# Performance work log

Hardware: AMD Instinct MI355X
Metric: run time of the kernel (lower is better)

The kernel has to match this reference:

```python
import jax, jax.numpy as jnp
import numpy as np
import math

BS, SEQ, HID = 1, 2048, 2048
NH, NKV, HD = 32, 8, 64
BASE = 10000.0


def rotate_half(x):
    x1, x2 = x[..., : x.shape[-1] // 2], x[..., x.shape[-1] // 2 :]
    return jnp.concatenate((-x2, x1), axis=-1)


def setup_inputs() -> dict:
    key = jax.random.key(0)
    ks = jax.random.split(key, 6)
    s = 0.02
    return {
        "x": jax.random.normal(ks[0], (BS, SEQ, HID), dtype=jnp.float32),
        "attention_mask": jnp.zeros((BS, SEQ), dtype=jnp.float32),
        "position_ids": jnp.broadcast_to(jnp.arange(SEQ, dtype=jnp.int64 if jax.config.jax_enable_x64 else jnp.int32), (BS, SEQ)),
        "wq": jax.random.normal(ks[1], (HID, NH * HD), dtype=jnp.float32) * s,
        "wk": jax.random.normal(ks[2], (HID, NKV * HD), dtype=jnp.float32) * s,
        "wv": jax.random.normal(ks[3], (HID, NKV * HD), dtype=jnp.float32) * s,
        "wo": jax.random.normal(ks[4], (NH * HD, HID), dtype=jnp.float32) * s,
    }


def reference(x, attention_mask, position_ids, wq, wk, wv, wo):
    bs, seq, _ = x.shape
    groups = NH // NKV

    q = (x @ wq).reshape(bs, seq, NH, HD).transpose(0, 2, 1, 3)   # [b,H,S,D]
    k = (x @ wk).reshape(bs, seq, NKV, HD).transpose(0, 2, 1, 3)  # [b,Hkv,S,D]
    v = (x @ wv).reshape(bs, seq, NKV, HD).transpose(0, 2, 1, 3)

    # rotary embedding
    inv_freq = 1.0 / (BASE ** (jnp.arange(0, HD, 2, dtype=jnp.float32) / HD))  # [D/2]
    freqs = position_ids.astype(jnp.float32)[:, :, None] * inv_freq[None, None, :]  # [b,S,D/2]
    emb = jnp.concatenate((freqs, freqs), axis=-1)               # [b,S,D]
    cos = jnp.cos(emb)[:, None, :, :].astype(x.dtype)            # [b,1,S,D]
    sin = jnp.sin(emb)[:, None, :, :].astype(x.dtype)
    q = q * cos + rotate_half(q) * sin
    k = k * cos + rotate_half(k) * sin

    # repeat_kv (GQA expand)
    k = jnp.repeat(k, groups, axis=1)  # [b,H,S,D]
    v = jnp.repeat(v, groups, axis=1)

    scores = jnp.einsum("bhqd,bhkd->bhqk", q, k) / math.sqrt(HD)
    scores = scores + attention_mask[:, None, None, :]
    attn = jax.nn.softmax(scores.astype(jnp.float32), axis=-1).astype(q.dtype)
    out = jnp.einsum("bhqk,bhkd->bhqd", attn, v)                 # [b,H,S,D]
    out = out.transpose(0, 2, 1, 3).reshape(bs, seq, NH * HD)
    return out @ wo
```

## Files before the change

### kernel.cpp

```cpp
#include <hip/hip_runtime.h>

#define SEQ 2048
#define HID 2048
#define NH  32
#define NKV 8
#define HD  64

typedef _Float16 f16;
typedef __attribute__((ext_vector_type(4))) _Float16 f16x4;
typedef __attribute__((ext_vector_type(8))) _Float16 f16x8;
typedef __attribute__((ext_vector_type(2))) __fp16   h16x2;
typedef __attribute__((ext_vector_type(4))) float    f32x4;

__device__ __forceinline__ f32x4 mfma_16x16x32(f16x8 a, f16x8 b, f32x4 c) {
    return __builtin_amdgcn_mfma_f32_16x16x32_f16(a, b, c, 0, 0, 0);
}

__device__ __forceinline__ void async16(const void* g, void* l) {
    __builtin_amdgcn_global_load_lds(
        (const __attribute__((address_space(1))) void*)g,
        (__attribute__((address_space(3))) void*)l,
        16, 0, 0);
}

__device__ __forceinline__ void xcd_colmap(int& bx, int& by) {
    int gx = gridDim.x, gy = gridDim.y;
    int nwg = gx * gy;
    int orig = by * gx + bx;
    int q = nwg >> 3, r = nwg & 7;
    int xcd = orig & 7, loc = orig >> 3;
    int wg = (xcd < r ? xcd * (q + 1) : r * (q + 1) + (xcd - r) * q) + loc;
    bx = wg / gy;
    by = wg - bx * gy;
}

__global__ void prep_all(const float* __restrict__ x,
                         const float* __restrict__ wq, const float* __restrict__ wk,
                         const float* __restrict__ wv, const float* __restrict__ wo,
                         f16* __restrict__ xb,
                         f16* __restrict__ Wcat, f16* __restrict__ woT) {
    __shared__ float tile[32][33];
    int z = blockIdx.z;
    int tx = threadIdx.x, ty = threadIdx.y;
    if (z == 4) {
        int idx = (blockIdx.y * 64 + blockIdx.x) * 256 + ty * 32 + tx;
        int i = idx * 4;
        float4 v = *(const float4*)(x + i);
        f16x4 o = { (f16)v.x, (f16)v.y, (f16)v.z, (f16)v.w };
        *(f16x4*)(xb + i) = o;
        return;
    }
    const float* src; f16* dst; int C;
    if      (z == 0) { src = wq; dst = Wcat;                         C = 2048; }
    else if (z == 1) { src = wk; dst = Wcat + (size_t)2048 * 2048;   C = 512;  }
    else if (z == 2) { src = wv; dst = Wcat + (size_t)2560 * 2048;   C = 512;  }
    else             { src = wo; dst = woT;                          C = 2048; }
    int c0 = blockIdx.x * 32, r0 = blockIdx.y * 32;
    if (c0 >= C) return;
#pragma unroll
    for (int i = 0; i < 32; i += 8)
        tile[ty + i][tx] = src[(size_t)(r0 + ty + i) * C + c0 + tx];
    __syncthreads();
#pragma unroll
    for (int i = 0; i < 32; i += 8)
        dst[(size_t)(c0 + ty + i) * 2048 + r0 + tx] = (f16)tile[tx][ty + i];
}

template <int MODE>
__global__ __launch_bounds__(256)
void gemm_bt(const f16* __restrict__ A, const f16* __restrict__ BT,
             float* __restrict__ Cf, f16* __restrict__ Q, f16* __restrict__ Kk,
             f16* __restrict__ VT, const int* __restrict__ pos,
             const float* __restrict__ mask, int N, int K) {
    __shared__ f16 As[2][64 * 64];
    __shared__ f16 Bs[2][128 * 64];
    int t = threadIdx.x;
    int w = t >> 6, lane = t & 63, quad = lane >> 4, l15 = lane & 15;
    int wm = w >> 1, wn = w & 1;
    int bx = blockIdx.x, by = blockIdx.y;
    xcd_colmap(bx, by);
    int m0 = by * 64, n0 = bx * 128;
    int sw = l15 & 7;

    int r8 = lane >> 3;
    int cc = (lane & 7) ^ r8;
    const f16* Ag0 = A  + (size_t)(m0 + w * 16 + r8) * K + cc * 8;
    const f16* Ag1 = Ag0 + (size_t)8 * K;
    const f16* Bg  = BT + (size_t)(n0 + w * 32 + r8) * K + cc * 8;

    f32x4 acc[2][4] = {};

    async16(Ag0, &As[0][w * 1024]);
    async16(Ag1, &As[0][w * 1024 + 512]);
#pragma unroll
    for (int g = 0; g < 4; g++)
        async16(Bg + (size_t)(8 * g) * K, &Bs[0][w * 2048 + g * 512]);
    __syncthreads();

    int b = 0;
    for (int kt = 64; kt <= K; kt += 64) {
        if (kt < K) {
            async16(Ag0 + kt, &As[b ^ 1][w * 1024]);
            async16(Ag1 + kt, &As[b ^ 1][w * 1024 + 512]);
#pragma unroll
            for (int g = 0; g < 4; g++)
                async16(Bg + (size_t)(8 * g) * K + kt, &Bs[b ^ 1][w * 2048 + g * 512]);
        }
        f16x8 af[2][2], bf[4][2];
#pragma unroll
        for (int mi = 0; mi < 2; mi++) {
            int row = wm * 32 + mi * 16 + l15;
#pragma unroll
            for (int kh = 0; kh < 2; kh++)
                af[mi][kh] = *(const f16x8*)(&As[b][row * 64 + ((kh * 4 + quad) ^ sw) * 8]);
        }
#pragma unroll
        for (int ni = 0; ni < 4; ni++) {
            int row = wn * 64 + ni * 16 + l15;
#pragma unroll
            for (int kh = 0; kh < 2; kh++)
                bf[ni][kh] = *(const f16x8*)(&Bs[b][row * 64 + ((kh * 4 + quad) ^ sw) * 8]);
        }
#pragma unroll
        for (int mi = 0; mi < 2; mi++)
#pragma unroll
            for (int ni = 0; ni < 4; ni++) {
                acc[mi][ni] = mfma_16x16x32(af[mi][0], bf[ni][0], acc[mi][ni]);
                acc[mi][ni] = mfma_16x16x32(af[mi][1], bf[ni][1], acc[mi][ni]);
            }
        __syncthreads();
        b ^= 1;
    }

    int rb  = m0 + wm * 32 + quad * 4;
    int cbh = n0 + wn * 64;
    if (MODE == 0) {
        if (cbh < (NH + NKV) * HD) {
            bool isQ = cbh < NH * HD;
            f16* dst = isQ ? (Q  + (size_t)(cbh >> 6) * SEQ * HD)
                           : (Kk + (size_t)((cbh - NH * HD) >> 6) * SEQ * HD);
            float scale = isQ ? 0.18033688011112042f : 1.0f;
            float fr[2];
#pragma unroll
            for (int ni = 0; ni < 2; ni++)
                fr[ni] = __builtin_amdgcn_exp2f(
                    (float)(ni * 16 + l15) * -0.41524101186092029f);
#pragma unroll
            for (int mi = 0; mi < 2; mi++)
#pragma unroll
                for (int r = 0; r < 4; r++) {
                    int row = rb + mi * 16 + r;
                    float pv = (float)pos[row];
#pragma unroll
                    for (int ni = 0; ni < 2; ni++) {
                        float sn, cs;
                        __sincosf(pv * fr[ni], &sn, &cs);
                        float x1 = acc[mi][ni][r], x2 = acc[mi][ni + 2][r];
                        int d = ni * 16 + l15;
                        dst[(size_t)row * HD + d]      = (f16)(scale * (x1 * cs - x2 * sn));
                        dst[(size_t)row * HD + d + 32] = (f16)(scale * (x2 * cs + x1 * sn));
                    }
                }
        } else {
            const float LOG2E = 1.4426950408889634f;
#pragma unroll
            for (int mi = 0; mi < 2; mi++) {
                float4 mv = *(const float4*)(mask + rb + mi * 16);
                float em[4];
#pragma unroll
                for (int r = 0; r < 4; r++)
                    em[r] = __builtin_amdgcn_exp2f((&mv.x)[r] * LOG2E);
#pragma unroll
                for (int ni = 0; ni < 4; ni++) {
                    int c2 = cbh - (NH + NKV) * HD + ni * 16 + l15;
                    f16x4 v4;
                    ((h16x2*)&v4)[0] = __builtin_amdgcn_cvt_pkrtz(
                        acc[mi][ni][0] * em[0], acc[mi][ni][1] * em[1]);
                    ((h16x2*)&v4)[1] = __builtin_amdgcn_cvt_pkrtz(
                        acc[mi][ni][2] * em[2], acc[mi][ni][3] * em[3]);
                    *(f16x4*)(VT + (size_t)c2 * SEQ + rb + mi * 16) = v4;
                }
            }
        }
    } else {
#pragma unroll
        for (int mi = 0; mi < 2; mi++)
#pragma unroll
            for (int ni = 0; ni < 4; ni++)
#pragma unroll
                for (int r = 0; r < 4; r++)
                    Cf[(size_t)(rb + mi * 16 + r) * N + cbh + ni * 16 + l15] =
                        acc[mi][ni][r];
    }
}

__global__ __launch_bounds__(512)
void attn_fused(const f16* __restrict__ Qb, const f16* __restrict__ Kb,
                const f16* __restrict__ VTb, const float* __restrict__ mask,
                f16* __restrict__ ctx) {
    __shared__ f16 Ks[2][64 * 64];
    __shared__ f16 Vs[2][64 * 64];
    __shared__ f16 Em[SEQ];

    int t = threadIdx.x, w = t >> 6, lane = t & 63, quad = lane >> 4, l15 = lane & 15;
    int h = blockIdx.y, kvh = h >> 2;
    int qbase = blockIdx.x * 256 + w * 32;
    const f16* Qh = Qb  + (size_t)h   * SEQ * HD;
    const f16* Kh = Kb  + (size_t)kvh * SEQ * HD;
    const f16* Vh = VTb + (size_t)kvh * HD * SEQ;
    int sw = l15 & 7;
    const float LOG2E = 1.4426950408889634f;

    int r8 = lane >> 3;
    int cc = (lane & 7) ^ r8;
    bool isK = w < 4;
    int ws = isK ? w : (w - 4);
    const f16* g0;
    long gstep;
    if (isK) {
        int gk = 32 * (ws >> 1) + 4 * (ws & 1) + 8 * (r8 >> 2) + (r8 & 3);
        g0 = Kh + (size_t)gk * HD + cc * 8;
        gstep = (long)16 * HD;
    } else {
        g0 = Vh + (size_t)(ws * 16 + r8) * SEQ + cc * 8;
        gstep = (long)8 * SEQ;
    }
    const f16* g1 = g0 + gstep;
    long adv = isK ? (long)64 * HD : 64;
    int lr0 = ws * 16 * 64, lr1 = lr0 + 8 * 64;

    {
        f16* dst = isK ? &Ks[0][0] : &Vs[0][0];
        async16(g0, dst + lr0);
        async16(g1, dst + lr1);
    }

    {
        float4 mv = *(const float4*)(mask + t * 4);
        f16x4 e;
        ((h16x2*)&e)[0] = __builtin_amdgcn_cvt_pkrtz(
            __builtin_amdgcn_exp2f(mv.x * LOG2E), __builtin_amdgcn_exp2f(mv.y * LOG2E));
        ((h16x2*)&e)[1] = __builtin_amdgcn_cvt_pkrtz(
            __builtin_amdgcn_exp2f(mv.z * LOG2E), __builtin_amdgcn_exp2f(mv.w * LOG2E));
        *(f16x4*)(&Em[t * 4]) = e;
    }

    f16x8 bq[2][2];
#pragma unroll
    for (int qg = 0; qg < 2; qg++)
#pragma unroll
        for (int ks = 0; ks < 2; ks++)
            bq[qg][ks] = *(const f16x8*)(Qh + (size_t)(qbase + qg * 16 + l15) * HD
                                            + ks * 32 + quad * 8);

    f32x4 o[4][2] = {};
    f32x4 ol[2]   = {};

    int c0 = (quad ^ sw) * 8, c1 = ((4 | quad) ^ sw) * 8;

    asm volatile("s_waitcnt lgkmcnt(0)" ::: "memory");

    int b = 0;
    const int NT = SEQ / 64;
    for (int ktl = 0; ktl < NT; ktl++) {
        if (ktl + 1 < NT) {
            g0 += adv; g1 += adv;
            f16* dst = isK ? &Ks[b ^ 1][0] : &Vs[b ^ 1][0];
            async16(g0, dst + lr0);
            async16(g1, dst + lr1);
            asm volatile("s_waitcnt vmcnt(2)" ::: "memory");
        } else {
            asm volatile("s_waitcnt vmcnt(0)" ::: "memory");
        }
        __builtin_amdgcn_s_barrier();
        __builtin_amdgcn_sched_barrier(0);

        const f16* Kb_ = &Ks[b][0];
        const f16* Vb_ = &Vs[b][0];

        f32x4 st[4][2] = {};
        __builtin_amdgcn_s_setprio(1);
#pragma unroll
        for (int ni = 0; ni < 4; ni++) {
            const f16* kr = Kb_ + (ni * 16 + l15) * 64;
            f16x8 ak0 = *(const f16x8*)(kr + c0);
            f16x8 ak1 = *(const f16x8*)(kr + c1);
#pragma unroll
            for (int qg = 0; qg < 2; qg++) {
                st[ni][qg] = mfma_16x16x32(ak0, bq[qg][0], st[ni][qg]);
                st[ni][qg] = mfma_16x16x32(ak1, bq[qg][1], st[ni][qg]);
            }
        }
        __builtin_amdgcn_s_setprio(0);
        f16x8 pb[2][2];
#pragma unroll
        for (int ni = 0; ni < 4; ni++)
#pragma unroll
            for (int qg = 0; qg < 2; qg++) {
                h16x2 lo = __builtin_amdgcn_cvt_pkrtz(
                    __builtin_amdgcn_exp2f(st[ni][qg][0]),
                    __builtin_amdgcn_exp2f(st[ni][qg][1]));
                h16x2 hi = __builtin_amdgcn_cvt_pkrtz(
                    __builtin_amdgcn_exp2f(st[ni][qg][2]),
                    __builtin_amdgcn_exp2f(st[ni][qg][3]));
                ((h16x2*)&pb[qg][ni >> 1])[(ni & 1) * 2]     = lo;
                ((h16x2*)&pb[qg][ni >> 1])[(ni & 1) * 2 + 1] = hi;
            }
        f16x8 em0 = *(const f16x8*)(&Em[ktl * 64 + quad * 8]);
        f16x8 em1 = *(const f16x8*)(&Em[ktl * 64 + 32 + quad * 8]);
        __builtin_amdgcn_s_setprio(1);
#pragma unroll
        for (int qg = 0; qg < 2; qg++) {
            ol[qg] = mfma_16x16x32(em0, pb[qg][0], ol[qg]);
            ol[qg] = mfma_16x16x32(em1, pb[qg][1], ol[qg]);
        }
#pragma unroll
        for (int dt = 0; dt < 4; dt++) {
            const f16* vr = Vb_ + (dt * 16 + l15) * 64;
            f16x8 av0 = *(const f16x8*)(vr + c0);
            f16x8 av1 = *(const f16x8*)(vr + c1);
#pragma unroll
            for (int qg = 0; qg < 2; qg++) {
                o[dt][qg] = mfma_16x16x32(av0, pb[qg][0], o[dt][qg]);
                o[dt][qg] = mfma_16x16x32(av1, pb[qg][1], o[dt][qg]);
            }
        }
        __builtin_amdgcn_s_setprio(0);
        __builtin_amdgcn_sched_barrier(0);
        __builtin_amdgcn_s_barrier();
        b ^= 1;
    }

    float inv[2] = { 1.0f / ol[0][0], 1.0f / ol[1][0] };
#pragma unroll
    for (int dt = 0; dt < 4; dt++)
#pragma unroll
        for (int qg = 0; qg < 2; qg++) {
            f16x4 v4;
            ((h16x2*)&v4)[0] = __builtin_amdgcn_cvt_pkrtz(
                o[dt][qg][0] * inv[qg], o[dt][qg][1] * inv[qg]);
            ((h16x2*)&v4)[1] = __builtin_amdgcn_cvt_pkrtz(
                o[dt][qg][2] * inv[qg], o[dt][qg][3] * inv[qg]);
            *(f16x4*)(ctx + (size_t)(qbase + qg * 16 + l15) * (NH * HD)
                          + h * HD + dt * 16 + quad * 4) = v4;
        }
}

extern "C" void kernel_launch(void* const* d_in, const int* in_sizes, int n_in,
                              void* d_out, int out_size, void* d_ws, size_t ws_size,
                              hipStream_t stream) {
    const float* x    = (const float*)d_in[0];
    const float* mask = (const float*)d_in[1];
    const int*   pos  = (const int*)  d_in[2];
    const float* wq   = (const float*)d_in[3];
    const float* wk   = (const float*)d_in[4];
    const float* wv   = (const float*)d_in[5];
    const float* wo   = (const float*)d_in[6];
    float* out = (float*)d_out;

    char* ws = (char*)d_ws;
    f16*   xb    = (f16*)(ws);
    f16*   Wcat  = (f16*)(ws + ((size_t)8  << 20));
    f16*   woT   = (f16*)(ws + ((size_t)20 << 20));
    f16*   Qb    = (f16*)(ws + ((size_t)28 << 20));
    f16*   Kb    = (f16*)(ws + ((size_t)36 << 20));
    f16*   VTb   = (f16*)(ws + ((size_t)38 << 20));
    f16*   ctx   = (f16*)(ws);

    prep_all<<<dim3(64, 64, 5), dim3(32, 8), 0, stream>>>(
        x, wq, wk, wv, wo, xb, Wcat, woT);

    gemm_bt<0><<<dim3(3072 / 128, 2048 / 64), 256, 0, stream>>>(
        xb, Wcat, nullptr, Qb, Kb, VTb, pos, mask, 3072, 2048);

    attn_fused<<<dim3(SEQ / 256, NH), 512, 0, stream>>>(
        Qb, Kb, VTb, mask, ctx);

    gemm_bt<1><<<dim3(2048 / 128, 2048 / 64), 256, 0, stream>>>(
        ctx, woT, out, nullptr, nullptr, nullptr, nullptr, nullptr, 2048, 2048);
}
```

Before: 204.6 us.

## Enlarge GEMM tiles to 128x128 and halve attention block size

The projection and output GEMMs now use 128x128 output tiles, with each wave computing a 64x64 sub-tile. Global-to-LDS loads are paced with explicit vmcnt waits and raw s_barrier, and the MFMA section is raised with setprio. Larger tiles give more operand reuse per LDS load but launch fewer blocks (256 to 384) on a 256-CU part and need more accumulator registers. The attention kernel moves from 512-thread blocks handling 256 queries to 256-thread blocks handling 128 queries, which doubles the block count for better CU occupancy; each loader wave now fetches 32 K/V rows with four async copies.

```diff
diff --git a/kernel.cpp b/kernel.cpp
--- a/kernel.cpp
+++ b/kernel.cpp
@@ -72,44 +72,49 @@
              float* __restrict__ Cf, f16* __restrict__ Q, f16* __restrict__ Kk,
              f16* __restrict__ VT, const int* __restrict__ pos,
              const float* __restrict__ mask, int N, int K) {
-    __shared__ f16 As[2][64 * 64];
+    __shared__ f16 As[2][128 * 64];
     __shared__ f16 Bs[2][128 * 64];
     int t = threadIdx.x;
     int w = t >> 6, lane = t & 63, quad = lane >> 4, l15 = lane & 15;
     int wm = w >> 1, wn = w & 1;
     int bx = blockIdx.x, by = blockIdx.y;
     xcd_colmap(bx, by);
-    int m0 = by * 64, n0 = bx * 128;
+    int m0 = by * 128, n0 = bx * 128;
     int sw = l15 & 7;
 
     int r8 = lane >> 3;
     int cc = (lane & 7) ^ r8;
-    const f16* Ag0 = A  + (size_t)(m0 + w * 16 + r8) * K + cc * 8;
-    const f16* Ag1 = Ag0 + (size_t)8 * K;
-    const f16* Bg  = BT + (size_t)(n0 + w * 32 + r8) * K + cc * 8;
-
-    f32x4 acc[2][4] = {};
-
-    async16(Ag0, &As[0][w * 1024]);
-    async16(Ag1, &As[0][w * 1024 + 512]);
-#pragma unroll
-    for (int g = 0; g < 4; g++)
-        async16(Bg + (size_t)(8 * g) * K, &Bs[0][w * 2048 + g * 512]);
+    const f16* Ag = A  + (size_t)(m0 + w * 32 + r8) * K + cc * 8;
+    const f16* Bg = BT + (size_t)(n0 + w * 32 + r8) * K + cc * 8;
+
+    f32x4 acc[4][4] = {};
+
+#pragma unroll
+    for (int a = 0; a < 4; a++) {
+        async16(Ag + (size_t)(8 * a) * K, &As[0][(w * 32 + 8 * a) * 64]);
+        async16(Bg + (size_t)(8 * a) * K, &Bs[0][(w * 32 + 8 * a) * 64]);
+    }
     __syncthreads();
 
     int b = 0;
     for (int kt = 64; kt <= K; kt += 64) {
         if (kt < K) {
-            async16(Ag0 + kt, &As[b ^ 1][w * 1024]);
-            async16(Ag1 + kt, &As[b ^ 1][w * 1024 + 512]);
-#pragma unroll
-            for (int g = 0; g < 4; g++)
-                async16(Bg + (size_t)(8 * g) * K + kt, &Bs[b ^ 1][w * 2048 + g * 512]);
-        }
-        f16x8 af[2][2], bf[4][2];
-#pragma unroll
-        for (int mi = 0; mi < 2; mi++) {
-            int row = wm * 32 + mi * 16 + l15;
+#pragma unroll
+            for (int a = 0; a < 4; a++) {
+                async16(Ag + (size_t)(8 * a) * K + kt, &As[b ^ 1][(w * 32 + 8 * a) * 64]);
+                async16(Bg + (size_t)(8 * a) * K + kt, &Bs[b ^ 1][(w * 32 + 8 * a) * 64]);
+            }
+            asm volatile("s_waitcnt vmcnt(8)" ::: "memory");
+        } else {
+            asm volatile("s_waitcnt vmcnt(0)" ::: "memory");
+        }
+        __builtin_amdgcn_s_barrier();
+        __builtin_amdgcn_sched_barrier(0);
+
+        f16x8 af[4][2], bf[4][2];
+#pragma unroll
+        for (int mi = 0; mi < 4; mi++) {
+            int row = wm * 64 + mi * 16 + l15;
 #pragma unroll
             for (int kh = 0; kh < 2; kh++)
                 af[mi][kh] = *(const f16x8*)(&As[b][row * 64 + ((kh * 4 + quad) ^ sw) * 8]);
@@ -121,18 +126,21 @@
             for (int kh = 0; kh < 2; kh++)
                 bf[ni][kh] = *(const f16x8*)(&Bs[b][row * 64 + ((kh * 4 + quad) ^ sw) * 8]);
         }
-#pragma unroll
-        for (int mi = 0; mi < 2; mi++)
+        __builtin_amdgcn_s_setprio(1);
+#pragma unroll
+        for (int mi = 0; mi < 4; mi++)
 #pragma unroll
             for (int ni = 0; ni < 4; ni++) {
                 acc[mi][ni] = mfma_16x16x32(af[mi][0], bf[ni][0], acc[mi][ni]);
                 acc[mi][ni] = mfma_16x16x32(af[mi][1], bf[ni][1], acc[mi][ni]);
             }
-        __syncthreads();
+        __builtin_amdgcn_s_setprio(0);
+        __builtin_amdgcn_sched_barrier(0);
+        __builtin_amdgcn_s_barrier();
         b ^= 1;
     }
 
-    int rb  = m0 + wm * 32 + quad * 4;
+    int rb  = m0 + wm * 64 + quad * 4;
     int cbh = n0 + wn * 64;
     if (MODE == 0) {
         if (cbh < (NH + NKV) * HD) {
@@ -146,7 +154,7 @@
                 fr[ni] = __builtin_amdgcn_exp2f(
                     (float)(ni * 16 + l15) * -0.41524101186092029f);
 #pragma unroll
-            for (int mi = 0; mi < 2; mi++)
+            for (int mi = 0; mi < 4; mi++)
 #pragma unroll
                 for (int r = 0; r < 4; r++) {
                     int row = rb + mi * 16 + r;
@@ -164,7 +172,7 @@
         } else {
             const float LOG2E = 1.4426950408889634f;
 #pragma unroll
-            for (int mi = 0; mi < 2; mi++) {
+            for (int mi = 0; mi < 4; mi++) {
                 float4 mv = *(const float4*)(mask + rb + mi * 16);
                 float em[4];
 #pragma unroll
@@ -184,7 +192,7 @@
         }
     } else {
 #pragma unroll
-        for (int mi = 0; mi < 2; mi++)
+        for (int mi = 0; mi < 4; mi++)
 #pragma unroll
             for (int ni = 0; ni < 4; ni++)
 #pragma unroll
@@ -194,7 +202,7 @@
     }
 }
 
-__global__ __launch_bounds__(512)
+__global__ __launch_bounds__(256)
 void attn_fused(const f16* __restrict__ Qb, const f16* __restrict__ Kb,
                 const f16* __restrict__ VTb, const float* __restrict__ mask,
                 f16* __restrict__ ctx) {
@@ -204,7 +212,7 @@
 
     int t = threadIdx.x, w = t >> 6, lane = t & 63, quad = lane >> 4, l15 = lane & 15;
     int h = blockIdx.y, kvh = h >> 2;
-    int qbase = blockIdx.x * 256 + w * 32;
+    int qbase = blockIdx.x * 128 + w * 32;
     const f16* Qh = Qb  + (size_t)h   * SEQ * HD;
     const f16* Kh = Kb  + (size_t)kvh * SEQ * HD;
     const f16* Vh = VTb + (size_t)kvh * HD * SEQ;
@@ -213,36 +221,43 @@
 
     int r8 = lane >> 3;
     int cc = (lane & 7) ^ r8;
-    bool isK = w < 4;
-    int ws = isK ? w : (w - 4);
-    const f16* g0;
-    long gstep;
+    bool isK = w < 2;
+    int ws2 = isK ? w : (w - 2);
+    int lbase = ws2 * 32 * 64;
+    const f16 *kv0, *kv1, *kv2, *kv3;
+    long adv;
     if (isK) {
-        int gk = 32 * (ws >> 1) + 4 * (ws & 1) + 8 * (r8 >> 2) + (r8 & 3);
-        g0 = Kh + (size_t)gk * HD + cc * 8;
-        gstep = (long)16 * HD;
+        const f16* bl = Kh + (size_t)(ws2 * 32 + 8 * (r8 >> 2) + (r8 & 3)) * HD + cc * 8;
+        kv0 = bl;            kv1 = bl + (size_t)16 * HD;
+        kv2 = bl + (size_t)4 * HD;  kv3 = bl + (size_t)20 * HD;
+        adv = (long)64 * HD;
     } else {
-        g0 = Vh + (size_t)(ws * 16 + r8) * SEQ + cc * 8;
-        gstep = (long)8 * SEQ;
-    }
-    const f16* g1 = g0 + gstep;
-    long adv = isK ? (long)64 * HD : 64;
-    int lr0 = ws * 16 * 64, lr1 = lr0 + 8 * 64;
+        const f16* bl = Vh + (size_t)(ws2 * 32 + r8) * SEQ + cc * 8;
+        kv0 = bl;                   kv1 = bl + (size_t)8 * SEQ;
+        kv2 = bl + (size_t)16 * SEQ; kv3 = bl + (size_t)24 * SEQ;
+        adv = 64;
+    }
 
     {
-        f16* dst = isK ? &Ks[0][0] : &Vs[0][0];
-        async16(g0, dst + lr0);
-        async16(g1, dst + lr1);
+        f16* dst = (isK ? &Ks[0][0] : &Vs[0][0]) + lbase;
+        async16(kv0, dst);       async16(kv1, dst + 512);
+        async16(kv2, dst + 1024); async16(kv3, dst + 1536);
     }
 
     {
-        float4 mv = *(const float4*)(mask + t * 4);
-        f16x4 e;
+        int idx = t * 8;
+        float4 ma = *(const float4*)(mask + idx);
+        float4 mb = *(const float4*)(mask + idx + 4);
+        f16x8 e;
         ((h16x2*)&e)[0] = __builtin_amdgcn_cvt_pkrtz(
-            __builtin_amdgcn_exp2f(mv.x * LOG2E), __builtin_amdgcn_exp2f(mv.y * LOG2E));
+            __builtin_amdgcn_exp2f(ma.x * LOG2E), __builtin_amdgcn_exp2f(ma.y * LOG2E));
         ((h16x2*)&e)[1] = __builtin_amdgcn_cvt_pkrtz(
-            __builtin_amdgcn_exp2f(mv.z * LOG2E), __builtin_amdgcn_exp2f(mv.w * LOG2E));
-        *(f16x4*)(&Em[t * 4]) = e;
+            __builtin_amdgcn_exp2f(ma.z * LOG2E), __builtin_amdgcn_exp2f(ma.w * LOG2E));
+        ((h16x2*)&e)[2] = __builtin_amdgcn_cvt_pkrtz(
+            __builtin_amdgcn_exp2f(mb.x * LOG2E), __builtin_amdgcn_exp2f(mb.y * LOG2E));
+        ((h16x2*)&e)[3] = __builtin_amdgcn_cvt_pkrtz(
+            __builtin_amdgcn_exp2f(mb.z * LOG2E), __builtin_amdgcn_exp2f(mb.w * LOG2E));
+        *(f16x8*)(&Em[idx]) = e;
     }
 
     f16x8 bq[2][2];
@@ -264,11 +279,11 @@
     const int NT = SEQ / 64;
     for (int ktl = 0; ktl < NT; ktl++) {
         if (ktl + 1 < NT) {
-            g0 += adv; g1 += adv;
-            f16* dst = isK ? &Ks[b ^ 1][0] : &Vs[b ^ 1][0];
-            async16(g0, dst + lr0);
-            async16(g1, dst + lr1);
-            asm volatile("s_waitcnt vmcnt(2)" ::: "memory");
+            kv0 += adv; kv1 += adv; kv2 += adv; kv3 += adv;
+            f16* dst = (isK ? &Ks[b ^ 1][0] : &Vs[b ^ 1][0]) + lbase;
+            async16(kv0, dst);        async16(kv1, dst + 512);
+            async16(kv2, dst + 1024); async16(kv3, dst + 1536);
+            asm volatile("s_waitcnt vmcnt(4)" ::: "memory");
         } else {
             asm volatile("s_waitcnt vmcnt(0)" ::: "memory");
         }
@@ -370,12 +385,12 @@
     prep_all<<<dim3(64, 64, 5), dim3(32, 8), 0, stream>>>(
         x, wq, wk, wv, wo, xb, Wcat, woT);
 
-    gemm_bt<0><<<dim3(3072 / 128, 2048 / 64), 256, 0, stream>>>(
+    gemm_bt<0><<<dim3(3072 / 128, 2048 / 128), 256, 0, stream>>>(
         xb, Wcat, nullptr, Qb, Kb, VTb, pos, mask, 3072, 2048);
 
-    attn_fused<<<dim3(SEQ / 256, NH), 512, 0, stream>>>(
+    attn_fused<<<dim3(SEQ / 128, NH), 256, 0, stream>>>(
         Qb, Kb, VTb, mask, ctx);
 
-    gemm_bt<1><<<dim3(2048 / 128, 2048 / 64), 256, 0, stream>>>(
+    gemm_bt<1><<<dim3(2048 / 128, 2048 / 128), 256, 0, stream>>>(
         ctx, woT, out, nullptr, nullptr, nullptr, nullptr, nullptr, 2048, 2048);
 }
```

Result: slower. 222.2 us (+8.6%).
